# Performance work log

Hardware: AMD Instinct MI355X
Metric: run time of the kernel (lower is better)

Reference implementation:

```python
import jax, jax.numpy as jnp
import numpy as np

B, T, F = 4, 1024, 64
H = (2048, 1024, 512, 256)
EPS = 1e-5


def setup_inputs() -> dict:
    key = jax.random.key(0)
    ks = jax.random.split(key, 20)
    def rn(k, shape, s=0.05):
        return jax.random.normal(k, shape, dtype=jnp.float32) * s
    inp = {
        "x": jax.random.normal(ks[0], (B, T, F), dtype=jnp.float32),
        "bn_w": jax.random.uniform(ks[1], (T,), dtype=jnp.float32, minval=0.5, maxval=1.5),
        "bn_b": rn(ks[2], (T,)),
    }
    ins = (F, H[0], H[1], H[2])
    for l in range(4):
        inp[f"w_ih{l+1}"] = rn(ks[3 + 4 * l], (4 * H[l], ins[l]))
        inp[f"w_hh{l+1}"] = rn(ks[4 + 4 * l], (4 * H[l], H[l]))
        inp[f"b_ih{l+1}"] = rn(ks[5 + 4 * l], (4 * H[l],))
        inp[f"b_hh{l+1}"] = rn(ks[6 + 4 * l], (4 * H[l],))
    return inp


def _cell(x, h, c, w_ih, w_hh, b_ih, b_hh):
    # PyTorch LSTMCell: gate order i, f, g, o
    g = x @ w_ih.T + b_ih + h @ w_hh.T + b_hh  # (4H,)
    i, f, gg, o = jnp.split(g, 4)
    i = jax.nn.sigmoid(i)
    f = jax.nn.sigmoid(f)
    o = jax.nn.sigmoid(o)
    gg = jnp.tanh(gg)
    c_new = f * c + i * gg
    h_new = o * jnp.tanh(c_new)
    return h_new, c_new


def reference(x, bn_w, bn_b,
              w_ih1, w_hh1, b_ih1, b_hh1,
              w_ih2, w_hh2, b_ih2, b_hh2,
              w_ih3, w_hh3, b_ih3, b_hh3,
              w_ih4, w_hh4, b_ih4, b_hh4):
    # BatchNorm1d(timesteps): x is (N, C=T, L=F); normalize per timestep channel
    # over (N, L) with batch statistics (training mode, biased variance).
    mean = x.mean(axis=(0, 2), keepdims=True)
    var = x.var(axis=(0, 2), keepdims=True)
    xn = (x - mean) * jax.lax.rsqrt(var + EPS)
    xn = xn * bn_w[None, :, None] + bn_b[None, :, None]

    # Original forward carries hidden across the batch loop -> one scan of B*T steps.
    xs = xn.reshape(B * T, F)

    def step(carry, xt):
        h1, c1, h2, c2, h3, c3, h4, c4 = carry
        h1, c1 = _cell(xt, h1, c1, w_ih1, w_hh1, b_ih1, b_hh1)
        h2, c2 = _cell(h1, h2, c2, w_ih2, w_hh2, b_ih2, b_hh2)
        h3, c3 = _cell(h2, h3, c3, w_ih3, w_hh3, b_ih3, b_hh3)  # dropout = identity (eval)
        h4, c4 = _cell(h3, h4, c4, w_ih4, w_hh4, b_ih4, b_hh4)
        return (h1, c1, h2, c2, h3, c3, h4, c4), h4

    init = tuple(jnp.zeros((h,), dtype=jnp.float32) for h in
                 (H[0], H[0], H[1], H[1], H[2], H[2], H[3], H[3]))
    _, h4s = jax.lax.scan(step, init, xs)  # (B*T, H4)
    return h4s.reshape(B, T * H[3])
```

## Files before the change

### kernel.cpp

```cpp
#include <hip/hip_runtime.h>
#include <cstddef>

#define NSTEP 4096
#define PIN4(v) asm volatile("" : "+v"((v).x), "+v"((v).y), "+v"((v).z), "+v"((v).w))
#define FMA4(W,V,A) { (A)=fmaf((W).x,(V).x,(A)); (A)=fmaf((W).y,(V).y,(A)); (A)=fmaf((W).z,(V).z,(A)); (A)=fmaf((W).w,(V).w,(A)); }

__device__ __forceinline__ float ldc(const float* p) {
  return __hip_atomic_load(p, __ATOMIC_RELAXED, __HIP_MEMORY_SCOPE_AGENT);
}
__device__ __forceinline__ void stc(float* p, float v) {
  __hip_atomic_store(p, v, __ATOMIC_RELAXED, __HIP_MEMORY_SCOPE_AGENT);
}

__global__ __launch_bounds__(256) void bn_kernel(const float* __restrict__ x,
                                                 const float* __restrict__ bn_w,
                                                 const float* __restrict__ bn_b,
                                                 float* __restrict__ xn)
{
  const int t   = blockIdx.x;
  const int tid = threadIdx.x;
  const int b   = tid >> 6;
  const int f   = tid & 63;
  const float v = x[((size_t)b * 1024 + t) * 64 + f];
  float s = v, ss = v * v;
  #pragma unroll
  for (int off = 32; off > 0; off >>= 1) {
    s  += __shfl_down(s, off);
    ss += __shfl_down(ss, off);
  }
  __shared__ float sh[8];
  const int w = tid >> 6;
  if ((tid & 63) == 0) { sh[w] = s; sh[4 + w] = ss; }
  __syncthreads();
  const float S    = sh[0] + sh[1] + sh[2] + sh[3];
  const float SS   = sh[4] + sh[5] + sh[6] + sh[7];
  const float mean = S * (1.0f / 256.0f);
  const float var  = SS * (1.0f / 256.0f) - mean * mean;
  const float inv  = rsqrtf(var + 1e-5f);
  const float scale = bn_w[t] * inv;
  const float shift = bn_b[t] - mean * scale;
  xn[((size_t)b * 1024 + t) * 64 + f] = v * scale + shift;
}

template<int NBLK>
__device__ __forceinline__ void grid_barrier(unsigned* __restrict__ bar,
                                             unsigned step1, int tid)
{
  constexpr unsigned GSZ = NBLK / 8;
  __syncthreads();
  if (tid == 0) {
    unsigned* gcnt = bar + 16 + 16 * (blockIdx.x / GSZ);
    unsigned* root = bar;
    const unsigned a = __hip_atomic_fetch_add(gcnt, 1u, __ATOMIC_RELAXED,
                                              __HIP_MEMORY_SCOPE_AGENT);
    if (a == step1 * GSZ - 1u)
      __hip_atomic_fetch_add(root, 1u, __ATOMIC_RELAXED, __HIP_MEMORY_SCOPE_AGENT);
    const unsigned tgt = step1 * 8u;
    while (__hip_atomic_load(root, __ATOMIC_RELAXED, __HIP_MEMORY_SCOPE_AGENT) < tgt)
      __builtin_amdgcn_s_sleep(2);
    asm volatile("" ::: "memory");
  }
  __syncthreads();
}

__device__ __forceinline__ void reduce4(float& a0, float& a1, float& a2, float& a3)
{
  #pragma unroll
  for (int off = 32; off; off >>= 1) {
    a0 += __shfl_xor(a0, off);
    a1 += __shfl_xor(a1, off);
    a2 += __shfl_xor(a2, off);
    a3 += __shfl_xor(a3, off);
  }
}

__device__ __forceinline__ float lstm_act4(float a0, float a1, float a2, float a3,
                                           float4 bs, float& c)
{
  const float ig = 1.0f / (1.0f + expf(-(a0 + bs.x)));
  const float fg = 1.0f / (1.0f + expf(-(a1 + bs.y)));
  const float og = 1.0f / (1.0f + expf(-(a3 + bs.w)));
  const float gt = tanhf(a2 + bs.z);
  c = fg * c + ig * gt;
  return og * tanhf(c);
}

#define L1J(j) { const float4 v = *(const float4*)&hbuf[(j)*256 + lane*4]; \
  FMA4(h0##j, v, a0); FMA4(h1##j, v, a1); FMA4(h2##j, v, a2); FMA4(h3##j, v, a3); }

__global__ __launch_bounds__(512)
__attribute__((amdgpu_waves_per_eu(2, 2)))
void lstm_l1(const float* __restrict__ win, const float* __restrict__ whh,
             const float* __restrict__ bih, const float* __restrict__ bhh,
             const float* __restrict__ X,
             float* __restrict__ Hout,
             unsigned* __restrict__ bar)
{
  constexpr int H = 2048;
  __shared__ __align__(16) float hbuf[2048];
  const int tid = threadIdx.x, lane = tid & 63, wsl = tid >> 6;
  const int hid = blockIdx.x * 8 + wsl;

  const size_t r0 = (size_t)0 * H + hid, r1 = (size_t)1 * H + hid,
               r2 = (size_t)2 * H + hid, r3 = (size_t)3 * H + hid;
  float4 wi = make_float4(win[r0 * 64 + lane], win[r1 * 64 + lane],
                          win[r2 * 64 + lane], win[r3 * 64 + lane]);
  PIN4(wi);
  const float4* p0 = (const float4*)(whh + r0 * H);
  const float4* p1 = (const float4*)(whh + r1 * H);
  const float4* p2 = (const float4*)(whh + r2 * H);
  const float4* p3 = (const float4*)(whh + r3 * H);
  float4 h00=p0[0*64+lane], h01=p0[1*64+lane], h02=p0[2*64+lane], h03=p0[3*64+lane],
         h04=p0[4*64+lane], h05=p0[5*64+lane], h06=p0[6*64+lane], h07=p0[7*64+lane];
  float4 h10=p1[0*64+lane], h11=p1[1*64+lane], h12=p1[2*64+lane], h13=p1[3*64+lane],
         h14=p1[4*64+lane], h15=p1[5*64+lane], h16=p1[6*64+lane], h17=p1[7*64+lane];
  float4 h20=p2[0*64+lane], h21=p2[1*64+lane], h22=p2[2*64+lane], h23=p2[3*64+lane],
         h24=p2[4*64+lane], h25=p2[5*64+lane], h26=p2[6*64+lane], h27=p2[7*64+lane];
  float4 h30=p3[0*64+lane], h31=p3[1*64+lane], h32=p3[2*64+lane], h33=p3[3*64+lane],
         h34=p3[4*64+lane], h35=p3[5*64+lane], h36=p3[6*64+lane], h37=p3[7*64+lane];
  PIN4(h00); PIN4(h01); PIN4(h02); PIN4(h03); PIN4(h04); PIN4(h05); PIN4(h06); PIN4(h07);
  PIN4(h10); PIN4(h11); PIN4(h12); PIN4(h13); PIN4(h14); PIN4(h15); PIN4(h16); PIN4(h17);
  PIN4(h20); PIN4(h21); PIN4(h22); PIN4(h23); PIN4(h24); PIN4(h25); PIN4(h26); PIN4(h27);
  PIN4(h30); PIN4(h31); PIN4(h32); PIN4(h33); PIN4(h34); PIN4(h35); PIN4(h36); PIN4(h37);
  float4 bs = make_float4(bih[r0] + bhh[r0], bih[r1] + bhh[r1],
                          bih[r2] + bhh[r2], bih[r3] + bhh[r3]);
  PIN4(bs);
  float c = 0.0f;

  #pragma unroll 1
  for (int t = 0; t < NSTEP; ++t) {
    {
      const float* hrow = Hout + (size_t)t * H;
      #pragma unroll
      for (int k = 0; k < 4; ++k) hbuf[tid + 512 * k] = ldc(hrow + tid + 512 * k);
    }
    __syncthreads();
    const float xv = X[(size_t)t * 64 + lane];
    float a0 = wi.x * xv, a1 = wi.y * xv, a2 = wi.z * xv, a3 = wi.w * xv;
    L1J(0) L1J(1) L1J(2) L1J(3) L1J(4) L1J(5) L1J(6) L1J(7)
    reduce4(a0, a1, a2, a3);
    const float hn = lstm_act4(a0, a1, a2, a3, bs, c);
    if (lane == 0) stc(&Hout[(size_t)(t + 1) * H + hid], hn);
    asm volatile("s_waitcnt vmcnt(0)" ::: "memory");
    grid_barrier<256>(bar, (unsigned)(t + 1), tid);
  }
}

#define L2XJ(j) { const float4 v = xr[(j)*64+lane]; \
  FMA4(i0##j,v,a0); FMA4(i1##j,v,a1); FMA4(i2##j,v,a2); FMA4(i3##j,v,a3); }
#define L2HJ(j) { const float4 v = *(const float4*)&hbuf[(j)*256+lane*4]; \
  FMA4(m0##j,v,a0); FMA4(m1##j,v,a1); FMA4(m2##j,v,a2); FMA4(m3##j,v,a3); }
#define L3XJ(j) { const float4 v = *(const float4*)&hbuf[(j)*256+lane*4]; \
  FMA4(d0##j,v,a0); FMA4(d1##j,v,a1); FMA4(d2##j,v,a2); FMA4(d3##j,v,a3); }
#define L3HJ(j) { const float4 v = *(const float4*)&hbuf[4096 + (j)*256+lane*4]; \
  FMA4(e0##j,v,a0); FMA4(e1##j,v,a1); FMA4(e2##j,v,a2); FMA4(e3##j,v,a3); }
#define L4XJ(j) { const float4 v = *(const float4*)&hbuf[(j)*256+lane*4]; \
  FMA4(f0##j,v,a0); FMA4(f1##j,v,a1); FMA4(f2##j,v,a2); FMA4(f3##j,v,a3); }

__global__ __launch_bounds__(512)
__attribute__((amdgpu_waves_per_eu(2, 2)))
void lstm_l234(const float* __restrict__ win2, const float* __restrict__ whh2,
               const float* __restrict__ bih2, const float* __restrict__ bhh2,
               const float* __restrict__ win3, const float* __restrict__ whh3,
               const float* __restrict__ bih3, const float* __restrict__ bhh3,
               const float* __restrict__ win4, const float* __restrict__ whh4,
               const float* __restrict__ bih4, const float* __restrict__ bhh4,
               const float* __restrict__ X2,
               float* __restrict__ H2t, float* __restrict__ H3t,
               float* __restrict__ H4t, float* __restrict__ out,
               unsigned* __restrict__ bar)
{
  __shared__ __align__(16) float hbuf[1536];
  const int tid = threadIdx.x, lane = tid & 63, wsl = tid >> 6;
  const int gw = blockIdx.x * 8 + wsl;
  const int role = (blockIdx.x < 128) ? 0 : ((blockIdx.x < 192) ? 1 : 2);

  if (role == 0) {
    const int hid = gw;
    const size_t R0 = hid, R1 = 1024 + hid, R2 = 2048 + hid, R3 = 3072 + hid;
    const float4* pi0 = (const float4*)(win2 + R0 * 2048);
    const float4* pi1 = (const float4*)(win2 + R1 * 2048);
    const float4* pi2 = (const float4*)(win2 + R2 * 2048);
    const float4* pi3 = (const float4*)(win2 + R3 * 2048);
    const float4* ph0 = (const float4*)(whh2 + R0 * 1024);
    const float4* ph1 = (const float4*)(whh2 + R1 * 1024);
    const float4* ph2 = (const float4*)(whh2 + R2 * 1024);
    const float4* ph3 = (const float4*)(whh2 + R3 * 1024);
    float4 i00=pi0[0*64+lane], i01=pi0[1*64+lane], i02=pi0[2*64+lane], i03=pi0[3*64+lane],
           i04=pi0[4*64+lane], i05=pi0[5*64+lane], i06=pi0[6*64+lane], i07=pi0[7*64+lane];
    float4 i10=pi1[0*64+lane], i11=pi1[1*64+lane], i12=pi1[2*64+lane], i13=pi1[3*64+lane],
           i14=pi1[4*64+lane], i15=pi1[5*64+lane], i16=pi1[6*64+lane], i17=pi1[7*64+lane];
    float4 i20=pi2[0*64+lane], i21=pi2[1*64+lane], i22=pi2[2*64+lane], i23=pi2[3*64+lane],
           i24=pi2[4*64+lane], i25=pi2[5*64+lane], i26=pi2[6*64+lane], i27=pi2[7*64+lane];
    float4 i30=pi3[0*64+lane], i31=pi3[1*64+lane], i32=pi3[2*64+lane], i33=pi3[3*64+lane],
           i34=pi3[4*64+lane], i35=pi3[5*64+lane], i36=pi3[6*64+lane], i37=pi3[7*64+lane];
    float4 m00=ph0[0*64+lane], m01=ph0[1*64+lane], m02=ph0[2*64+lane], m03=ph0[3*64+lane];
    float4 m10=ph1[0*64+lane], m11=ph1[1*64+lane], m12=ph1[2*64+lane], m13=ph1[3*64+lane];
    float4 m20=ph2[0*64+lane], m21=ph2[1*64+lane], m22=ph2[2*64+lane], m23=ph2[3*64+lane];
    float4 m30=ph3[0*64+lane], m31=ph3[1*64+lane], m32=ph3[2*64+lane], m33=ph3[3*64+lane];
    PIN4(i00); PIN4(i01); PIN4(i02); PIN4(i03); PIN4(i04); PIN4(i05); PIN4(i06); PIN4(i07);
    PIN4(i10); PIN4(i11); PIN4(i12); PIN4(i13); PIN4(i14); PIN4(i15); PIN4(i16); PIN4(i17);
    PIN4(i20); PIN4(i21); PIN4(i22); PIN4(i23); PIN4(i24); PIN4(i25); PIN4(i26); PIN4(i27);
    PIN4(i30); PIN4(i31); PIN4(i32); PIN4(i33); PIN4(i34); PIN4(i35); PIN4(i36); PIN4(i37);
    PIN4(m00); PIN4(m01); PIN4(m02); PIN4(m03);
    PIN4(m10); PIN4(m11); PIN4(m12); PIN4(m13);
    PIN4(m20); PIN4(m21); PIN4(m22); PIN4(m23);
    PIN4(m30); PIN4(m31); PIN4(m32); PIN4(m33);
    float4 bs = make_float4(bih2[R0] + bhh2[R0], bih2[R1] + bhh2[R1],
                            bih2[R2] + bhh2[R2], bih2[R3] + bhh2[R3]);
    PIN4(bs);
    float c = 0.0f;
    #pragma unroll 1
    for (int s = 0; s < NSTEP + 2; ++s) {
      if (s < NSTEP) {
        {
          const float* hrow = H2t + (size_t)s * 1024;
          #pragma unroll
          for (int k = 0; k < 2; ++k) hbuf[tid + 512 * k] = ldc(hrow + tid + 512 * k);
        }
        __syncthreads();
        const float4* xr = (const float4*)(X2 + (size_t)s * 2048);
        float a0 = 0.f, a1 = 0.f, a2 = 0.f, a3 = 0.f;
        L2XJ(0) L2XJ(1) L2XJ(2) L2XJ(3) L2XJ(4) L2XJ(5) L2XJ(6) L2XJ(7)
        L2HJ(0) L2HJ(1) L2HJ(2) L2HJ(3)
        reduce4(a0, a1, a2, a3);
        const float hn = lstm_act4(a0, a1, a2, a3, bs, c);
        if (lane == 0) stc(&H2t[(size_t)(s + 1) * 1024 + hid], hn);
        asm volatile("s_waitcnt vmcnt(0)" ::: "memory");
      }
      grid_barrier<224>(bar, (unsigned)(s + 1), tid);
    }
  } else if (role == 1) {
    const int hid = gw - 1024;
    const float* X3 = H2t + 1024;
    const size_t R0 = hid, R1 = 512 + hid, R2 = 1024 + hid, R3 = 1536 + hid;
    const float4* pi0 = (const float4*)(win3 + R0 * 1024);
    const float4* pi1 = (const float4*)(win3 + R1 * 1024);
    const float4* pi2 = (const float4*)(win3 + R2 * 1024);
    const float4* pi3 = (const float4*)(win3 + R3 * 1024);
    const float4* ph0 = (const float4*)(whh3 + R0 * 512);
    const float4* ph1 = (const float4*)(whh3 + R1 * 512);
    const float4* ph2 = (const float4*)(whh3 + R2 * 512);
    const float4* ph3 = (const float4*)(whh3 + R3 * 512);
    float4 d00=pi0[0*64+lane], d01=pi0[1*64+lane], d02=pi0[2*64+lane], d03=pi0[3*64+lane];
    float4 d10=pi1[0*64+lane], d11=pi1[1*64+lane], d12=pi1[2*64+lane], d13=pi1[3*64+lane];
    float4 d20=pi2[0*64+lane], d21=pi2[1*64+lane], d22=pi2[2*64+lane], d23=pi2[3*64+lane];
    float4 d30=pi3[0*64+lane], d31=pi3[1*64+lane], d32=pi3[2*64+lane], d33=pi3[3*64+lane];
    float4 e00=ph0[0*64+lane], e01=ph0[1*64+lane];
    float4 e10=ph1[0*64+lane], e11=ph1[1*64+lane];
    float4 e20=ph2[0*64+lane], e21=ph2[1*64+lane];
    float4 e30=ph3[0*64+lane], e31=ph3[1*64+lane];
    PIN4(d00); PIN4(d01); PIN4(d02); PIN4(d03);
    PIN4(d10); PIN4(d11); PIN4(d12); PIN4(d13);
    PIN4(d20); PIN4(d21); PIN4(d22); PIN4(d23);
    PIN4(d30); PIN4(d31); PIN4(d32); PIN4(d33);
    PIN4(e00); PIN4(e01); PIN4(e10); PIN4(e11);
    PIN4(e20); PIN4(e21); PIN4(e30); PIN4(e31);
    float4 bs = make_float4(bih3[R0] + bhh3[R0], bih3[R1] + bhh3[R1],
                            bih3[R2] + bhh3[R2], bih3[R3] + bhh3[R3]);
    PIN4(bs);
    float c = 0.0f;
    #pragma unroll 1
    for (int s = 0; s < NSTEP + 2; ++s) {
      if (s >= 1 && s <= NSTEP) {
        const int t3 = s - 1;
        {
          const float* xrow = X3  + (size_t)t3 * 1024;
          const float* hrow = H3t + (size_t)t3 * 512;
          #pragma unroll
          for (int k = 0; k < 2; ++k) hbuf[tid + 512 * k] = ldc(xrow + tid + 512 * k);
          hbuf[1024 + tid] = ldc(hrow + tid);
        }
        __syncthreads();
        float a0 = 0.f, a1 = 0.f, a2 = 0.f, a3 = 0.f;
        L3XJ(0) L3XJ(1) L3XJ(2) L3XJ(3)
        {
          const float4 v = *(const float4*)&hbuf[1024 + 0*256 + lane*4];
          FMA4(e00,v,a0); FMA4(e10,v,a1); FMA4(e20,v,a2); FMA4(e30,v,a3);
        }
        {
          const float4 v = *(const float4*)&hbuf[1024 + 1*256 + lane*4];
          FMA4(e01,v,a0); FMA4(e11,v,a1); FMA4(e21,v,a2); FMA4(e31,v,a3);
        }
        reduce4(a0, a1, a2, a3);
        const float hn = lstm_act4(a0, a1, a2, a3, bs, c);
        if (lane == 0) stc(&H3t[(size_t)(t3 + 1) * 512 + hid], hn);
        asm volatile("s_waitcnt vmcnt(0)" ::: "memory");
      }
      grid_barrier<224>(bar, (unsigned)(s + 1), tid);
    }
  } else {
    const int hid = gw - 1536;
    const float* X4 = H3t + 512;
    const size_t R0 = hid, R1 = 256 + hid, R2 = 512 + hid, R3 = 768 + hid;
    const float4* pi0 = (const float4*)(win4 + R0 * 512);
    const float4* pi1 = (const float4*)(win4 + R1 * 512);
    const float4* pi2 = (const float4*)(win4 + R2 * 512);
    const float4* pi3 = (const float4*)(win4 + R3 * 512);
    const float4* ph0 = (const float4*)(whh4 + R0 * 256);
    const float4* ph1 = (const float4*)(whh4 + R1 * 256);
    const float4* ph2 = (const float4*)(whh4 + R2 * 256);
    const float4* ph3 = (const float4*)(whh4 + R3 * 256);
    float4 f00=pi0[0*64+lane], f01=pi0[1*64+lane];
    float4 f10=pi1[0*64+lane], f11=pi1[1*64+lane];
    float4 f20=pi2[0*64+lane], f21=pi2[1*64+lane];
    float4 f30=pi3[0*64+lane], f31=pi3[1*64+lane];
    float4 g0=ph0[lane], g1=ph1[lane], g2=ph2[lane], g3=ph3[lane];
    PIN4(f00); PIN4(f01); PIN4(f10); PIN4(f11);
    PIN4(f20); PIN4(f21); PIN4(f30); PIN4(f31);
    PIN4(g0); PIN4(g1); PIN4(g2); PIN4(g3);
    float4 bs = make_float4(bih4[R0] + bhh4[R0], bih4[R1] + bhh4[R1],
                            bih4[R2] + bhh4[R2], bih4[R3] + bhh4[R3]);
    PIN4(bs);
    float c = 0.0f;
    #pragma unroll 1
    for (int s = 0; s < NSTEP + 2; ++s) {
      if (s >= 2) {
        const int t4 = s - 2;
        {
          const float* xrow = X4  + (size_t)t4 * 512;
          const float* hrow = H4t + (size_t)t4 * 256;
          hbuf[tid] = ldc(xrow + tid);
          if (tid < 256) hbuf[512 + tid] = ldc(hrow + tid);
        }
        __syncthreads();
        float a0 = 0.f, a1 = 0.f, a2 = 0.f, a3 = 0.f;
        L4XJ(0) L4XJ(1)
        {
          const float4 v = *(const float4*)&hbuf[512 + lane*4];
          FMA4(g0,v,a0); FMA4(g1,v,a1); FMA4(g2,v,a2); FMA4(g3,v,a3);
        }
        reduce4(a0, a1, a2, a3);
        const float hn = lstm_act4(a0, a1, a2, a3, bs, c);
        if (lane == 0) {
          stc(&H4t[(size_t)(t4 + 1) * 256 + hid], hn);
          out[(size_t)t4 * 256 + hid] = hn;
        }
        asm volatile("s_waitcnt vmcnt(0)" ::: "memory");
      }
      grid_barrier<224>(bar, (unsigned)(s + 1), tid);
    }
  }
}

struct Params {
  const float* xn;
  const float* w_ih[4];
  const float* w_hh[4];
  const float* b_ih[4];
  const float* b_hh[4];
  float* h[4];
  float* c[4];
  float* out;
  int s;
};

__global__ __launch_bounds__(256) void step_kernel(Params p)
{
  const int lane = threadIdx.x & 63;
  const int W = blockIdx.x * 4 + (threadIdx.x >> 6);

  int layer, h, H, IN, t;
  if (W < 2048)      { layer = 0; h = W;        H = 2048; IN = 64;   t = p.s;     }
  else if (W < 3072) { layer = 1; h = W - 2048; H = 1024; IN = 2048; t = p.s - 1; }
  else if (W < 3584) { layer = 2; h = W - 3072; H = 512;  IN = 1024; t = p.s - 2; }
  else               { layer = 3; h = W - 3584; H = 256;  IN = 512;  t = p.s - 3; }
  if (t < 0 || t >= NSTEP) return;

  const float* xin;
  if (layer == 0) xin = p.xn + (size_t)t * 64;
  else            xin = p.h[layer - 1] + (size_t)(t & 1) * IN;
  const float* hprev = p.h[layer] + (size_t)((t + 1) & 1) * H;
  float*       hout  = p.h[layer] + (size_t)(t & 1) * H;
  const float* wih = p.w_ih[layer];
  const float* whh = p.w_hh[layer];

  float acc[4];
  #pragma unroll
  for (int g = 0; g < 4; ++g) {
    const size_t r = (size_t)g * H + h;
    const float* wi = wih + r * IN;
    const float* wh = whh + r * (size_t)H;
    float a = 0.0f;
    for (int k = lane; k < IN; k += 64) a += wi[k] * xin[k];
    for (int k = lane; k < H;  k += 64) a += wh[k] * hprev[k];
    acc[g] = a;
  }
  #pragma unroll
  for (int off = 32; off > 0; off >>= 1) {
    #pragma unroll
    for (int g = 0; g < 4; ++g) acc[g] += __shfl_down(acc[g], off);
  }
  if (lane == 0) {
    const float* bi = p.b_ih[layer];
    const float* bh = p.b_hh[layer];
    const float gi = acc[0] + bi[h]         + bh[h];
    const float gf = acc[1] + bi[H + h]     + bh[H + h];
    const float gg = acc[2] + bi[2 * H + h] + bh[2 * H + h];
    const float go = acc[3] + bi[3 * H + h] + bh[3 * H + h];
    const float ig = 1.0f / (1.0f + expf(-gi));
    const float fg = 1.0f / (1.0f + expf(-gf));
    const float og = 1.0f / (1.0f + expf(-go));
    const float gt = tanhf(gg);
    const float cn = fg * p.c[layer][h] + ig * gt;
    const float hn = og * tanhf(cn);
    p.c[layer][h] = cn;
    hout[h] = hn;
    if (layer == 3) p.out[(size_t)t * 256 + h] = hn;
  }
}

extern "C" void kernel_launch(void* const* d_in, const int* in_sizes, int n_in,
                              void* d_out, int out_size, void* d_ws, size_t ws_size,
                              hipStream_t stream)
{
  const float* x    = (const float*)d_in[0];
  const float* bn_w = (const float*)d_in[1];
  const float* bn_b = (const float*)d_in[2];
  const float* wih[4]; const float* whh[4]; const float* bih[4]; const float* bhh[4];
  for (int l = 0; l < 4; ++l) {
    wih[l] = (const float*)d_in[3 + 4 * l];
    whh[l] = (const float*)d_in[4 + 4 * l];
    bih[l] = (const float*)d_in[5 + 4 * l];
    bhh[l] = (const float*)d_in[6 + 4 * l];
  }
  float* out = (float*)d_out;

  const size_t XN  = (size_t)NSTEP * 64;
  const size_t NH1 = (size_t)(NSTEP + 1) * 2048;
  const size_t NH2 = (size_t)(NSTEP + 1) * 1024;
  const size_t NH3 = (size_t)(NSTEP + 1) * 512;
  const size_t NH4 = (size_t)(NSTEP + 1) * 256;
  const size_t need = 4096 + (XN + NH1 + NH2 + NH3 + NH4) * sizeof(float);

  if (ws_size >= need) {
    unsigned* bar = (unsigned*)d_ws;
    float* fb = (float*)((char*)d_ws + 4096);
    float* xn = fb;
    float* H1 = xn + XN;
    float* H2 = H1 + NH1;
    float* H3 = H2 + NH2;
    float* H4 = H3 + NH3;

    hipMemsetAsync(bar, 0, 4096, stream);
    hipMemsetAsync(H1, 0, 2048 * sizeof(float), stream);
    hipMemsetAsync(H2, 0, 1024 * sizeof(float), stream);
    hipMemsetAsync(H3, 0,  512 * sizeof(float), stream);
    hipMemsetAsync(H4, 0,  256 * sizeof(float), stream);

    bn_kernel<<<1024, 256, 0, stream>>>(x, bn_w, bn_b, xn);

    lstm_l1<<<256, 512, 0, stream>>>(wih[0], whh[0], bih[0], bhh[0],
                                     xn, H1, bar);

    lstm_l234<<<224, 512, 0, stream>>>(wih[1], whh[1], bih[1], bhh[1],
                                       wih[2], whh[2], bih[2], bhh[2],
                                       wih[3], whh[3], bih[3], bhh[3],
                                       H1 + 2048, H2, H3, H4, out, bar + 256);
    return;
  }

  Params p;
  for (int l = 0; l < 4; ++l) { p.w_ih[l] = wih[l]; p.w_hh[l] = whh[l];
                                p.b_ih[l] = bih[l]; p.b_hh[l] = bhh[l]; }
  float* ws = (float*)d_ws;
  float* xn = ws;
  float* st = ws + (size_t)NSTEP * 64;
  p.xn = xn;
  const int Hs[4] = {2048, 1024, 512, 256};
  float* cur = st;
  for (int l = 0; l < 4; ++l) { p.h[l] = cur; cur += 2 * Hs[l]; }
  for (int l = 0; l < 4; ++l) { p.c[l] = cur; cur += Hs[l]; }
  p.out = out;

  const size_t state_bytes = (size_t)(cur - st) * sizeof(float);
  hipMemsetAsync(st, 0, state_bytes, stream);
  bn_kernel<<<1024, 256, 0, stream>>>(x, bn_w, bn_b, xn);
  for (int s = 0; s < NSTEP + 3; ++s) {
    p.s = s;
    step_kernel<<<960, 256, 0, stream>>>(p);
  }
}
```

Baseline: 53.48 ms.

## Fuse all four LSTM layers into one persistent wavefront-pipelined kernel

Replaces the two sequential persistent kernels (layer 1 over all steps, then layers 2-4) with one 480-block persistent kernel. Each layer runs one step behind the layer below, so all four layers work concurrently under a single shared grid barrier. Layer 2 now stages its input row into LDS instead of reading it from global memory. The barrier is regrouped into 16 counters with a shorter sleep. This removes the serial layer-1 pass, but every step now waits on a barrier across 480 blocks, and it relies on all blocks being co-resident (launch bounds 512,4), which risks deadlock if they are not.

```diff
diff --git a/kernel.cpp b/kernel.cpp
--- a/kernel.cpp
+++ b/kernel.cpp
@@ -42,11 +42,12 @@
   xn[((size_t)b * 1024 + t) * 64 + f] = v * scale + shift;
 }
 
-template<int NBLK>
+template<int NBLK, int GROUPS>
 __device__ __forceinline__ void grid_barrier(unsigned* __restrict__ bar,
                                              unsigned step1, int tid)
 {
-  constexpr unsigned GSZ = NBLK / 8;
+  constexpr unsigned GSZ = NBLK / GROUPS;
+  static_assert(NBLK % GROUPS == 0, "grouping");
   __syncthreads();
   if (tid == 0) {
     unsigned* gcnt = bar + 16 + 16 * (blockIdx.x / GSZ);
@@ -55,9 +56,9 @@
                                               __HIP_MEMORY_SCOPE_AGENT);
     if (a == step1 * GSZ - 1u)
       __hip_atomic_fetch_add(root, 1u, __ATOMIC_RELAXED, __HIP_MEMORY_SCOPE_AGENT);
-    const unsigned tgt = step1 * 8u;
+    const unsigned tgt = step1 * (unsigned)GROUPS;
     while (__hip_atomic_load(root, __ATOMIC_RELAXED, __HIP_MEMORY_SCOPE_AGENT) < tgt)
-      __builtin_amdgcn_s_sleep(2);
+      __builtin_amdgcn_s_sleep(1);
     asm volatile("" ::: "memory");
   }
   __syncthreads();
@@ -85,98 +86,85 @@
   return og * tanhf(c);
 }
 
-#define L1J(j) { const float4 v = *(const float4*)&hbuf[(j)*256 + lane*4]; \
+#define L1J(j)  { const float4 v = *(const float4*)&hbuf[(j)*256 + lane*4]; \
   FMA4(h0##j, v, a0); FMA4(h1##j, v, a1); FMA4(h2##j, v, a2); FMA4(h3##j, v, a3); }
-
-__global__ __launch_bounds__(512)
-__attribute__((amdgpu_waves_per_eu(2, 2)))
-void lstm_l1(const float* __restrict__ win, const float* __restrict__ whh,
-             const float* __restrict__ bih, const float* __restrict__ bhh,
-             const float* __restrict__ X,
-             float* __restrict__ Hout,
-             unsigned* __restrict__ bar)
-{
-  constexpr int H = 2048;
-  __shared__ __align__(16) float hbuf[2048];
-  const int tid = threadIdx.x, lane = tid & 63, wsl = tid >> 6;
-  const int hid = blockIdx.x * 8 + wsl;
-
-  const size_t r0 = (size_t)0 * H + hid, r1 = (size_t)1 * H + hid,
-               r2 = (size_t)2 * H + hid, r3 = (size_t)3 * H + hid;
-  float4 wi = make_float4(win[r0 * 64 + lane], win[r1 * 64 + lane],
-                          win[r2 * 64 + lane], win[r3 * 64 + lane]);
-  PIN4(wi);
-  const float4* p0 = (const float4*)(whh + r0 * H);
-  const float4* p1 = (const float4*)(whh + r1 * H);
-  const float4* p2 = (const float4*)(whh + r2 * H);
-  const float4* p3 = (const float4*)(whh + r3 * H);
-  float4 h00=p0[0*64+lane], h01=p0[1*64+lane], h02=p0[2*64+lane], h03=p0[3*64+lane],
-         h04=p0[4*64+lane], h05=p0[5*64+lane], h06=p0[6*64+lane], h07=p0[7*64+lane];
-  float4 h10=p1[0*64+lane], h11=p1[1*64+lane], h12=p1[2*64+lane], h13=p1[3*64+lane],
-         h14=p1[4*64+lane], h15=p1[5*64+lane], h16=p1[6*64+lane], h17=p1[7*64+lane];
-  float4 h20=p2[0*64+lane], h21=p2[1*64+lane], h22=p2[2*64+lane], h23=p2[3*64+lane],
-         h24=p2[4*64+lane], h25=p2[5*64+lane], h26=p2[6*64+lane], h27=p2[7*64+lane];
-  float4 h30=p3[0*64+lane], h31=p3[1*64+lane], h32=p3[2*64+lane], h33=p3[3*64+lane],
-         h34=p3[4*64+lane], h35=p3[5*64+lane], h36=p3[6*64+lane], h37=p3[7*64+lane];
-  PIN4(h00); PIN4(h01); PIN4(h02); PIN4(h03); PIN4(h04); PIN4(h05); PIN4(h06); PIN4(h07);
-  PIN4(h10); PIN4(h11); PIN4(h12); PIN4(h13); PIN4(h14); PIN4(h15); PIN4(h16); PIN4(h17);
-  PIN4(h20); PIN4(h21); PIN4(h22); PIN4(h23); PIN4(h24); PIN4(h25); PIN4(h26); PIN4(h27);
-  PIN4(h30); PIN4(h31); PIN4(h32); PIN4(h33); PIN4(h34); PIN4(h35); PIN4(h36); PIN4(h37);
-  float4 bs = make_float4(bih[r0] + bhh[r0], bih[r1] + bhh[r1],
-                          bih[r2] + bhh[r2], bih[r3] + bhh[r3]);
-  PIN4(bs);
-  float c = 0.0f;
-
-  #pragma unroll 1
-  for (int t = 0; t < NSTEP; ++t) {
-    {
-      const float* hrow = Hout + (size_t)t * H;
-      #pragma unroll
-      for (int k = 0; k < 4; ++k) hbuf[tid + 512 * k] = ldc(hrow + tid + 512 * k);
-    }
-    __syncthreads();
-    const float xv = X[(size_t)t * 64 + lane];
-    float a0 = wi.x * xv, a1 = wi.y * xv, a2 = wi.z * xv, a3 = wi.w * xv;
-    L1J(0) L1J(1) L1J(2) L1J(3) L1J(4) L1J(5) L1J(6) L1J(7)
-    reduce4(a0, a1, a2, a3);
-    const float hn = lstm_act4(a0, a1, a2, a3, bs, c);
-    if (lane == 0) stc(&Hout[(size_t)(t + 1) * H + hid], hn);
-    asm volatile("s_waitcnt vmcnt(0)" ::: "memory");
-    grid_barrier<256>(bar, (unsigned)(t + 1), tid);
-  }
-}
-
-#define L2XJ(j) { const float4 v = xr[(j)*64+lane]; \
+#define L2XJ(j) { const float4 v = *(const float4*)&hbuf[(j)*256+lane*4]; \
   FMA4(i0##j,v,a0); FMA4(i1##j,v,a1); FMA4(i2##j,v,a2); FMA4(i3##j,v,a3); }
-#define L2HJ(j) { const float4 v = *(const float4*)&hbuf[(j)*256+lane*4]; \
+#define L2HJ(j) { const float4 v = *(const float4*)&hbuf[2048 + (j)*256+lane*4]; \
   FMA4(m0##j,v,a0); FMA4(m1##j,v,a1); FMA4(m2##j,v,a2); FMA4(m3##j,v,a3); }
 #define L3XJ(j) { const float4 v = *(const float4*)&hbuf[(j)*256+lane*4]; \
   FMA4(d0##j,v,a0); FMA4(d1##j,v,a1); FMA4(d2##j,v,a2); FMA4(d3##j,v,a3); }
-#define L3HJ(j) { const float4 v = *(const float4*)&hbuf[4096 + (j)*256+lane*4]; \
-  FMA4(e0##j,v,a0); FMA4(e1##j,v,a1); FMA4(e2##j,v,a2); FMA4(e3##j,v,a3); }
 #define L4XJ(j) { const float4 v = *(const float4*)&hbuf[(j)*256+lane*4]; \
   FMA4(f0##j,v,a0); FMA4(f1##j,v,a1); FMA4(f2##j,v,a2); FMA4(f3##j,v,a3); }
 
-__global__ __launch_bounds__(512)
-__attribute__((amdgpu_waves_per_eu(2, 2)))
-void lstm_l234(const float* __restrict__ win2, const float* __restrict__ whh2,
-               const float* __restrict__ bih2, const float* __restrict__ bhh2,
-               const float* __restrict__ win3, const float* __restrict__ whh3,
-               const float* __restrict__ bih3, const float* __restrict__ bhh3,
-               const float* __restrict__ win4, const float* __restrict__ whh4,
-               const float* __restrict__ bih4, const float* __restrict__ bhh4,
-               const float* __restrict__ X2,
-               float* __restrict__ H2t, float* __restrict__ H3t,
-               float* __restrict__ H4t, float* __restrict__ out,
-               unsigned* __restrict__ bar)
-{
-  __shared__ __align__(16) float hbuf[1536];
+__global__ __launch_bounds__(512, 4)
+void lstm_all(const float* __restrict__ win1, const float* __restrict__ whh1,
+              const float* __restrict__ bih1, const float* __restrict__ bhh1,
+              const float* __restrict__ win2, const float* __restrict__ whh2,
+              const float* __restrict__ bih2, const float* __restrict__ bhh2,
+              const float* __restrict__ win3, const float* __restrict__ whh3,
+              const float* __restrict__ bih3, const float* __restrict__ bhh3,
+              const float* __restrict__ win4, const float* __restrict__ whh4,
+              const float* __restrict__ bih4, const float* __restrict__ bhh4,
+              const float* __restrict__ X,
+              float* __restrict__ H1t,
+              float* __restrict__ H2t, float* __restrict__ H3t,
+              float* __restrict__ H4t, float* __restrict__ out,
+              unsigned* __restrict__ bar)
+{
+  __shared__ __align__(16) float hbuf[3072];
   const int tid = threadIdx.x, lane = tid & 63, wsl = tid >> 6;
-  const int gw = blockIdx.x * 8 + wsl;
-  const int role = (blockIdx.x < 128) ? 0 : ((blockIdx.x < 192) ? 1 : 2);
-
-  if (role == 0) {
-    const int hid = gw;
+  const int blk = blockIdx.x;
+
+  if (blk < 256) {
+    constexpr int H = 2048;
+    const int hid = blk * 8 + wsl;
+    const size_t r0 = hid, r1 = H + hid, r2 = 2 * H + hid, r3 = 3 * H + hid;
+    float4 wi = make_float4(win1[r0 * 64 + lane], win1[r1 * 64 + lane],
+                            win1[r2 * 64 + lane], win1[r3 * 64 + lane]);
+    PIN4(wi);
+    const float4* p0 = (const float4*)(whh1 + r0 * H);
+    const float4* p1 = (const float4*)(whh1 + r1 * H);
+    const float4* p2 = (const float4*)(whh1 + r2 * H);
+    const float4* p3 = (const float4*)(whh1 + r3 * H);
+    float4 h00=p0[0*64+lane], h01=p0[1*64+lane], h02=p0[2*64+lane], h03=p0[3*64+lane],
+           h04=p0[4*64+lane], h05=p0[5*64+lane], h06=p0[6*64+lane], h07=p0[7*64+lane];
+    float4 h10=p1[0*64+lane], h11=p1[1*64+lane], h12=p1[2*64+lane], h13=p1[3*64+lane],
+           h14=p1[4*64+lane], h15=p1[5*64+lane], h16=p1[6*64+lane], h17=p1[7*64+lane];
+    float4 h20=p2[0*64+lane], h21=p2[1*64+lane], h22=p2[2*64+lane], h23=p2[3*64+lane],
+           h24=p2[4*64+lane], h25=p2[5*64+lane], h26=p2[6*64+lane], h27=p2[7*64+lane];
+    float4 h30=p3[0*64+lane], h31=p3[1*64+lane], h32=p3[2*64+lane], h33=p3[3*64+lane],
+           h34=p3[4*64+lane], h35=p3[5*64+lane], h36=p3[6*64+lane], h37=p3[7*64+lane];
+    PIN4(h00); PIN4(h01); PIN4(h02); PIN4(h03); PIN4(h04); PIN4(h05); PIN4(h06); PIN4(h07);
+    PIN4(h10); PIN4(h11); PIN4(h12); PIN4(h13); PIN4(h14); PIN4(h15); PIN4(h16); PIN4(h17);
+    PIN4(h20); PIN4(h21); PIN4(h22); PIN4(h23); PIN4(h24); PIN4(h25); PIN4(h26); PIN4(h27);
+    PIN4(h30); PIN4(h31); PIN4(h32); PIN4(h33); PIN4(h34); PIN4(h35); PIN4(h36); PIN4(h37);
+    float4 bs = make_float4(bih1[r0] + bhh1[r0], bih1[r1] + bhh1[r1],
+                            bih1[r2] + bhh1[r2], bih1[r3] + bhh1[r3]);
+    PIN4(bs);
+    float c = 0.0f;
+    #pragma unroll 1
+    for (int s = 0; s < NSTEP + 3; ++s) {
+      if (s < NSTEP) {
+        {
+          const float* hrow = H1t + (size_t)s * H;
+          #pragma unroll
+          for (int k = 0; k < 4; ++k) hbuf[tid + 512 * k] = ldc(hrow + tid + 512 * k);
+        }
+        __syncthreads();
+        const float xv = X[(size_t)s * 64 + lane];
+        float a0 = wi.x * xv, a1 = wi.y * xv, a2 = wi.z * xv, a3 = wi.w * xv;
+        L1J(0) L1J(1) L1J(2) L1J(3) L1J(4) L1J(5) L1J(6) L1J(7)
+        reduce4(a0, a1, a2, a3);
+        const float hn = lstm_act4(a0, a1, a2, a3, bs, c);
+        if (lane == 0) stc(&H1t[(size_t)(s + 1) * H + hid], hn);
+        asm volatile("s_waitcnt vmcnt(0)" ::: "memory");
+      }
+      grid_barrier<480, 16>(bar, (unsigned)(s + 1), tid);
+    }
+  } else if (blk < 384) {
+    const int hid = (blk - 256) * 8 + wsl;
+    const float* X2 = H1t + 2048;
     const size_t R0 = hid, R1 = 1024 + hid, R2 = 2048 + hid, R3 = 3072 + hid;
     const float4* pi0 = (const float4*)(win2 + R0 * 2048);
     const float4* pi1 = (const float4*)(win2 + R1 * 2048);
@@ -211,27 +199,30 @@
     PIN4(bs);
     float c = 0.0f;
     #pragma unroll 1
-    for (int s = 0; s < NSTEP + 2; ++s) {
-      if (s < NSTEP) {
-        {
-          const float* hrow = H2t + (size_t)s * 1024;
+    for (int s = 0; s < NSTEP + 3; ++s) {
+      if (s >= 1 && s <= NSTEP) {
+        const int t2 = s - 1;
+        {
+          const float* xrow = X2  + (size_t)t2 * 2048;
+          const float* hrow = H2t + (size_t)t2 * 1024;
           #pragma unroll
-          for (int k = 0; k < 2; ++k) hbuf[tid + 512 * k] = ldc(hrow + tid + 512 * k);
+          for (int k = 0; k < 4; ++k) hbuf[tid + 512 * k] = ldc(xrow + tid + 512 * k);
+          #pragma unroll
+          for (int k = 0; k < 2; ++k) hbuf[2048 + tid + 512 * k] = ldc(hrow + tid + 512 * k);
         }
         __syncthreads();
-        const float4* xr = (const float4*)(X2 + (size_t)s * 2048);
         float a0 = 0.f, a1 = 0.f, a2 = 0.f, a3 = 0.f;
         L2XJ(0) L2XJ(1) L2XJ(2) L2XJ(3) L2XJ(4) L2XJ(5) L2XJ(6) L2XJ(7)
         L2HJ(0) L2HJ(1) L2HJ(2) L2HJ(3)
         reduce4(a0, a1, a2, a3);
         const float hn = lstm_act4(a0, a1, a2, a3, bs, c);
-        if (lane == 0) stc(&H2t[(size_t)(s + 1) * 1024 + hid], hn);
+        if (lane == 0) stc(&H2t[(size_t)(t2 + 1) * 1024 + hid], hn);
         asm volatile("s_waitcnt vmcnt(0)" ::: "memory");
       }
-      grid_barrier<224>(bar, (unsigned)(s + 1), tid);
+      grid_barrier<480, 16>(bar, (unsigned)(s + 1), tid);
     }
-  } else if (role == 1) {
-    const int hid = gw - 1024;
+  } else if (blk < 448) {
+    const int hid = (blk - 384) * 8 + wsl;
     const float* X3 = H2t + 1024;
     const size_t R0 = hid, R1 = 512 + hid, R2 = 1024 + hid, R3 = 1536 + hid;
     const float4* pi0 = (const float4*)(win3 + R0 * 1024);
@@ -261,9 +252,9 @@
     PIN4(bs);
     float c = 0.0f;
     #pragma unroll 1
-    for (int s = 0; s < NSTEP + 2; ++s) {
-      if (s >= 1 && s <= NSTEP) {
-        const int t3 = s - 1;
+    for (int s = 0; s < NSTEP + 3; ++s) {
+      if (s >= 2 && s <= NSTEP + 1) {
+        const int t3 = s - 2;
         {
           const float* xrow = X3  + (size_t)t3 * 1024;
           const float* hrow = H3t + (size_t)t3 * 512;
@@ -287,10 +278,10 @@
         if (lane == 0) stc(&H3t[(size_t)(t3 + 1) * 512 + hid], hn);
         asm volatile("s_waitcnt vmcnt(0)" ::: "memory");
       }
-      grid_barrier<224>(bar, (unsigned)(s + 1), tid);
+      grid_barrier<480, 16>(bar, (unsigned)(s + 1), tid);
     }
   } else {
-    const int hid = gw - 1536;
+    const int hid = (blk - 448) * 8 + wsl;
     const float* X4 = H3t + 512;
     const size_t R0 = hid, R1 = 256 + hid, R2 = 512 + hid, R3 = 768 + hid;
     const float4* pi0 = (const float4*)(win4 + R0 * 512);
@@ -314,9 +305,9 @@
     PIN4(bs);
     float c = 0.0f;
     #pragma unroll 1
-    for (int s = 0; s < NSTEP + 2; ++s) {
-      if (s >= 2) {
-        const int t4 = s - 2;
+    for (int s = 0; s < NSTEP + 3; ++s) {
+      if (s >= 3) {
+        const int t4 = s - 3;
         {
           const float* xrow = X4  + (size_t)t4 * 512;
           const float* hrow = H4t + (size_t)t4 * 256;
@@ -338,7 +329,7 @@
         }
         asm volatile("s_waitcnt vmcnt(0)" ::: "memory");
       }
-      grid_barrier<224>(bar, (unsigned)(s + 1), tid);
+      grid_barrier<480, 16>(bar, (unsigned)(s + 1), tid);
     }
   }
 }
@@ -450,13 +441,11 @@
 
     bn_kernel<<<1024, 256, 0, stream>>>(x, bn_w, bn_b, xn);
 
-    lstm_l1<<<256, 512, 0, stream>>>(wih[0], whh[0], bih[0], bhh[0],
-                                     xn, H1, bar);
-
-    lstm_l234<<<224, 512, 0, stream>>>(wih[1], whh[1], bih[1], bhh[1],
-                                       wih[2], whh[2], bih[2], bhh[2],
-                                       wih[3], whh[3], bih[3], bhh[3],
-                                       H1 + 2048, H2, H3, H4, out, bar + 256);
+    lstm_all<<<480, 512, 0, stream>>>(wih[0], whh[0], bih[0], bhh[0],
+                                      wih[1], whh[1], bih[1], bhh[1],
+                                      wih[2], whh[2], bih[2], bhh[2],
+                                      wih[3], whh[3], bih[3], bhh[3],
+                                      xn, H1, H2, H3, H4, out, bar);
     return;
   }
 
```

Result: slower. 131.9 ms (+146.6%).
